# Optimization experiments

Measured on AMD Instinct MI355X. Metric: run time of the kernel, lower is better.

The kernel has to match this reference:

```python
import jax, jax.numpy as jnp
import numpy as np

B, H, W, C = 2, 64, 64, 256
G, K, L = 16, 9, 2
Cg = C // G


def _ln(x, g, b, eps=1e-6):
    m = jnp.mean(x, -1, keepdims=True)
    v = jnp.mean((x - m) ** 2, -1, keepdims=True)
    return (x - m) * jax.lax.rsqrt(v + eps) * g + b


def _conv(x, w, b=None, groups=1):
    y = jax.lax.conv_general_dilated(x, w, (1, 1), 'SAME',
        dimension_numbers=('NHWC', 'HWIO', 'NHWC'), feature_group_count=groups)
    return y if b is None else y + b


def _gelu(x):
    return jax.nn.gelu(x, approximate=False)  # torch nn.GELU (exact erf)


def _dcnv3(x, dw_w, dw_b, dwn_g, dwn_b, off_w, off_b, msk_w, msk_b,
           inp_w, inp_b, out_w, out_b, offset_scale=1.0):
    # x: [B,H,W,C] channels-last. kernel=3, stride=1, pad=1, dilation=1.
    xp = x @ inp_w + inp_b                                   # input_proj
    f = _gelu(_ln(_conv(x, dw_w, dw_b, groups=C), dwn_g, dwn_b))  # dw_conv branch
    off = (f @ off_w + off_b).reshape(B, H, W, G, K, 2) * offset_scale  # pixel units (x,y)
    mask = jax.nn.softmax((f @ msk_w + msk_b).reshape(B, H, W, G, K), axis=-1)
    dy, dx = jnp.meshgrid(jnp.arange(3.0) - 1.0, jnp.arange(3.0) - 1.0, indexing='ij')
    gx = dx.reshape(-1)
    gy = dy.reshape(-1)  # [K] kernel dilation grid
    # sampling locations in the zero-padded (pad=1) frame; pixel i center = i+0.5
    loc_x = (jnp.arange(W, dtype=x.dtype) + 1.5)[None, None, :, None, None] + gx + off[..., 0]
    loc_y = (jnp.arange(H, dtype=x.dtype) + 1.5)[None, :, None, None, None] + gy + off[..., 1]
    xg = jnp.pad(xp, ((0, 0), (1, 1), (1, 1), (0, 0))).reshape(B, H + 2, W + 2, G, Cg)
    px = loc_x - 0.5
    py = loc_y - 0.5
    x0 = jnp.floor(px).astype(jnp.int32)
    y0 = jnp.floor(py).astype(jnp.int32)
    fx = (px - x0)[..., None]
    fy = (py - y0)[..., None]
    Hp, Wp = H + 2, W + 2
    bi = jnp.arange(B).reshape(B, 1, 1, 1, 1)
    gi = jnp.arange(G).reshape(1, 1, 1, G, 1)

    def gather(yi, xi):  # zero padding outside bounds (grid_sample padding_mode='zeros')
        ok = ((yi >= 0) & (yi < Hp) & (xi >= 0) & (xi < Wp)).astype(x.dtype)[..., None]
        return xg[bi, jnp.clip(yi, 0, Hp - 1), jnp.clip(xi, 0, Wp - 1), gi] * ok

    top = gather(y0, x0) * (1 - fx) + gather(y0, x0 + 1) * fx
    bot = gather(y0 + 1, x0) * (1 - fx) + gather(y0 + 1, x0 + 1) * fx
    samp = top * (1 - fy) + bot * fy                         # [B,H,W,G,K,Cg]
    out = (samp * mask[..., None]).sum(4).reshape(B, H, W, C)
    return out @ out_w + out_b                               # output_proj


def _leffn(x, dc_w, dc_b, g, b, c1_w, c1_b, c2_w, c2_b, gamma):
    y = _ln(_conv(x, dc_w, dc_b, groups=C), g, b)
    y = _gelu(y @ c1_w + c1_b) @ c2_w + c2_b
    return x + gamma * y


def _cbam(x, w1, w2, sa_w, g, b):
    fc = lambda v: jax.nn.relu(v @ w1) @ w2
    ca = jax.nn.sigmoid(fc(x.mean((1, 2))) + fc(x.max((1, 2))))[:, None, None, :]
    x = x * ca
    sm = jnp.stack([x.mean(-1), x.max(-1)], -1)              # [B,H,W,2]
    x = x * jax.nn.sigmoid(_conv(sm, sa_w))
    return _ln(x, g, b)


def _upsample(x, w, bb, g, bt):
    y = jax.image.resize(x, (B, 2 * H, 2 * W, C), 'bilinear')  # align_corners=False
    y = _conv(y, w, bb)                                        # 3x3, C -> C//2
    return _gelu(_ln(y, g, bt))


def _forward(x, ln1_g, ln1_b, dw_w, dw_b, dwn_g, dwn_b, off_w, off_b, msk_w, msk_b,
             inp_w, inp_b, out_w, out_b, ln2_g, ln2_b, dc_w, dc_b, fn_g, fn_b,
             c1_w, c1_b, c2_w, c2_b, ffn_gamma, ca_w1, ca_w2, sa_w, cb_g, cb_b,
             nf_g, nf_b, up_w, up_b, up_g, up_bt):
    x = _cbam(x, ca_w1, ca_w2, sa_w, cb_g, cb_b)
    for i in range(L):  # fixed small depth; structural loop
        x = x + _dcnv3(_ln(x, ln1_g[i], ln1_b[i]), dw_w[i], dw_b[i], dwn_g[i], dwn_b[i],
                       off_w[i], off_b[i], msk_w[i], msk_b[i], inp_w[i], inp_b[i],
                       out_w[i], out_b[i])
        x = x + _leffn(_ln(x, ln2_g[i], ln2_b[i]), dc_w[i], dc_b[i], fn_g[i], fn_b[i],
                       c1_w[i], c1_b[i], c2_w[i], c2_b[i], ffn_gamma[i])
    x = _ln(x, nf_g, nf_b)
    return _upsample(x, up_w, up_b, up_g, up_bt)


def setup_inputs() -> dict:
    ks = iter(jax.random.split(jax.random.key(0), 80))
    r = lambda shp, s=0.02: jax.random.normal(next(ks), shp, dtype=jnp.float32) * s
    one = lambda shp: jnp.ones(shp, jnp.float32)
    zero = lambda shp: jnp.zeros(shp, jnp.float32)
    return dict(
        x=jax.random.normal(next(ks), (B, H, W, C), dtype=jnp.float32),
        ln1_g=one((L, C)), ln1_b=zero((L, C)),
        dw_w=r((L, 3, 3, 1, C)), dw_b=zero((L, C)),
        dwn_g=one((L, C)), dwn_b=zero((L, C)),
        off_w=r((L, C, G * K * 2), 0.01), off_b=zero((L, G * K * 2)),
        msk_w=r((L, C, G * K)), msk_b=zero((L, G * K)),
        inp_w=r((L, C, C)), inp_b=zero((L, C)),
        out_w=r((L, C, C)), out_b=zero((L, C)),
        ln2_g=one((L, C)), ln2_b=zero((L, C)),
        dc_w=r((L, 7, 7, 1, C)), dc_b=zero((L, C)),
        fn_g=one((L, C)), fn_b=zero((L, C)),
        c1_w=r((L, C, 4 * C)), c1_b=zero((L, 4 * C)),
        c2_w=r((L, 4 * C, C)), c2_b=zero((L, C)),
        ffn_gamma=0.7 * one((L, C)),
        ca_w1=r((C, C // 16)), ca_w2=r((C // 16, C)),
        sa_w=r((7, 7, 2, 1)),
        cb_g=one((C,)), cb_b=zero((C,)),
        nf_g=one((C,)), nf_b=zero((C,)),
        up_w=r((3, 3, C, C // 2)), up_b=zero((C // 2,)),
        up_g=one((C // 2,)), up_bt=zero((C // 2,)),
    )


def reference(x, ln1_g, ln1_b, dw_w, dw_b, dwn_g, dwn_b, off_w, off_b, msk_w, msk_b,
              inp_w, inp_b, out_w, out_b, ln2_g, ln2_b, dc_w, dc_b, fn_g, fn_b,
              c1_w, c1_b, c2_w, c2_b, ffn_gamma, ca_w1, ca_w2, sa_w, cb_g, cb_b,
              nf_g, nf_b, up_w, up_b, up_g, up_bt):
    return _forward(x, ln1_g, ln1_b, dw_w, dw_b, dwn_g, dwn_b, off_w, off_b, msk_w, msk_b,
                    inp_w, inp_b, out_w, out_b, ln2_g, ln2_b, dc_w, dc_b, fn_g, fn_b,
                    c1_w, c1_b, c2_w, c2_b, ffn_gamma, ca_w1, ca_w2, sa_w, cb_g, cb_b,
                    nf_g, nf_b, up_w, up_b, up_g, up_bt)
```

## Files before the change

### kernel.cpp

```cpp
#include <hip/hip_runtime.h>
#include <math.h>

#define B_ 2
#define H_ 64
#define W_ 64
#define C_ 256
#define G_ 16
#define HW_ (H_*W_)
#define M_ (B_*HW_)
#define C4_ (4*C_)
#define OFFN_ 288
#define MSKN_ 144
#define OMN_ 432
#define UH_ 128
#define UW_ 128
#define MUP_ (B_*UH_*UW_)
#define KUP_ (9*C_)
#define NOUT_ 128

typedef short short8 __attribute__((ext_vector_type(8)));
typedef float f32x4 __attribute__((ext_vector_type(4)));
typedef unsigned short us4 __attribute__((ext_vector_type(4)));

__device__ __forceinline__ float gelu_f(float x){
  return 0.5f * x * (1.f + erff(x * 0.70710678118654752440f));
}
__device__ __forceinline__ float sigmoid_f(float x){ return 1.f/(1.f+expf(-x)); }
__device__ __forceinline__ unsigned short f2bf(float x){
  unsigned int u = __float_as_uint(x);
  unsigned int r = (u + 0x7fffu + ((u>>16)&1u)) >> 16;
  return (unsigned short)r;
}
__device__ __forceinline__ float bf2f(unsigned short u){
  return __uint_as_float(((unsigned int)u) << 16);
}
__device__ __forceinline__ float bfl(unsigned int u){ return __uint_as_float(u<<16); }
__device__ __forceinline__ float bfh(unsigned int u){ return __uint_as_float(u & 0xffff0000u); }
__device__ __forceinline__ unsigned int pk(float a, float b){
  return (unsigned int)f2bf(a) | ((unsigned int)f2bf(b) << 16);
}

__device__ __forceinline__ void block_sum2(float& s, float& ss, float* sm){
  #pragma unroll
  for (int off=32; off>0; off>>=1){ s += __shfl_down(s, off); ss += __shfl_down(ss, off); }
  int lane = threadIdx.x & 63, wid = threadIdx.x >> 6;
  if (lane == 0){ sm[wid] = s; sm[4+wid] = ss; }
  __syncthreads();
  float a = 0.f, b = 0.f;
  int nw = blockDim.x >> 6;
  for (int i=0;i<nw;i++){ a += sm[i]; b += sm[4+i]; }
  s = a; ss = b;
}

__device__ __forceinline__ void block_summax(float& s, float& m, float* sm){
  #pragma unroll
  for (int off=32; off>0; off>>=1){ s += __shfl_down(s, off); m = fmaxf(m, __shfl_down(m, off)); }
  int lane = threadIdx.x & 63, wid = threadIdx.x >> 6;
  if (lane == 0){ sm[wid] = s; sm[4+wid] = m; }
  __syncthreads();
  float a = 0.f, b = -3.4e38f;
  int nw = blockDim.x >> 6;
  for (int i=0;i<nw;i++){ a += sm[i]; b = fmaxf(b, sm[4+i]); }
  s = a; m = b;
}

#define NJOBS 13
struct WtJobs {
  const float* src[NJOBS];
  unsigned short* dst[NJOBS];
  int Kd[NJOBS], Nd[NJOBS];
  int tOff[NJOBS+1];
};

__global__ __launch_bounds__(256) void k_wt_all(WtJobs J){
  __shared__ float tile[32][33];
  int bid = blockIdx.x;
  int j = 0;
  while (bid >= J.tOff[j+1]) j++;
  int lt = bid - J.tOff[j];
  const float* W = J.src[j];
  unsigned short* Wt = J.dst[j];
  int Kd = J.Kd[j], Nd = J.Nd[j];
  int ktiles = Kd >> 5;
  int k0 = (lt % ktiles) * 32, n0 = (lt / ktiles) * 32;
  int t = threadIdx.x;
  int r = t>>3, c4 = (t&7)*4;
  float4 v = make_float4(0.f,0.f,0.f,0.f);
  if (n0 + c4 < Nd) v = *(const float4*)(W + (size_t)(k0+r)*Nd + n0 + c4);
  tile[c4+0][r]=v.x; tile[c4+1][r]=v.y; tile[c4+2][r]=v.z; tile[c4+3][r]=v.w;
  __syncthreads();
  if (n0 + r < Nd){
    us4 o;
    o.x = f2bf(tile[r][c4+0]); o.y = f2bf(tile[r][c4+1]);
    o.z = f2bf(tile[r][c4+2]); o.w = f2bf(tile[r][c4+3]);
    *(us4*)(Wt + (size_t)(n0+r)*Kd + k0 + c4) = o;
  }
}

__global__ __launch_bounds__(256) void k_chpool(const float* __restrict__ Xin,
      float* __restrict__ psum, float* __restrict__ pmax){
  int chunk = blockIdx.x, b = blockIdx.y; int c = threadIdx.x;
  const float* p = Xin + (((size_t)b*HW_) + chunk*32)*C_ + c;
  float s = 0.f, m = -3.4e38f;
  for (int i=0;i<32;i++){ float v = p[(size_t)i*C_]; s += v; m = fmaxf(m, v); }
  psum[(b*128+chunk)*C_+c] = s; pmax[(b*128+chunk)*C_+c] = m;
}

__global__ __launch_bounds__(512) void k_ca(const float* __restrict__ psum, const float* __restrict__ pmax,
    const float* __restrict__ w1, const float* __restrict__ w2, float* __restrict__ ca){
  __shared__ float pm[2][256], px[2][256], hh[2][2][16];
  int t = threadIdx.x;
  {
    int b = t >> 8, c = t & 255;
    float s = 0.f, m = -3.4e38f;
    for (int ch=0; ch<128; ch++){ s += psum[(b*128+ch)*256+c]; m = fmaxf(m, pmax[(b*128+ch)*256+c]); }
    pm[b][c] = s * (1.f/4096.f); px[b][c] = m;
  }
  __syncthreads();
  if (t < 64){
    int b = t >> 5, typ = (t >> 4) & 1, j = t & 15;
    const float* src = typ ? px[b] : pm[b];
    float a = 0.f;
    for (int c2=0;c2<256;c2++) a += src[c2]*w1[c2*16+j];
    hh[b][typ][j] = fmaxf(a, 0.f);
  }
  __syncthreads();
  {
    int b = t >> 8, c = t & 255;
    float a = 0.f;
    for (int j=0;j<16;j++) a += (hh[b][0][j]+hh[b][1][j]) * w2[j*256+c];
    ca[b*256+c] = sigmoid_f(a);
  }
}

__global__ __launch_bounds__(256) void k_apply_ca(const float* __restrict__ Xin, float* __restrict__ X,
    const float* __restrict__ ca, float* __restrict__ smean, float* __restrict__ smax){
  __shared__ float sm[12];
  int pix = blockIdx.x, c = threadIdx.x;
  int b = pix >> 12;
  float v = Xin[(size_t)pix*C_+c] * ca[b*C_+c];
  X[(size_t)pix*C_+c] = v;
  float s = v, m = v;
  block_summax(s, m, sm);
  if (c == 0){ smean[pix] = s * (1.f/C_); smax[pix] = m; }
}

__global__ __launch_bounds__(256) void k_sa(const float* __restrict__ smean, const float* __restrict__ smax,
    const float* __restrict__ w, float* __restrict__ sa){
  int pix = blockIdx.x*256 + threadIdx.x;
  if (pix >= M_) return;
  int b = pix >> 12, hw = pix & 4095, h = hw >> 6, ww = hw & 63;
  float s = 0.f;
  for (int ky=0;ky<7;ky++){
    int hh = h + ky - 3; if (hh < 0 || hh >= H_) continue;
    for (int kx=0;kx<7;kx++){
      int xx = ww + kx - 3; if (xx < 0 || xx >= W_) continue;
      int q = (b<<12) + (hh<<6) + xx;
      s += smean[q]*w[(ky*7+kx)*2+0] + smax[q]*w[(ky*7+kx)*2+1];
    }
  }
  sa[pix] = sigmoid_f(s);
}

__global__ __launch_bounds__(256) void k_mul_ln(float* __restrict__ X, const float* __restrict__ sa,
    const float* __restrict__ g, const float* __restrict__ b){
  __shared__ float sm[12];
  int pix = blockIdx.x, c = threadIdx.x;
  float v = X[(size_t)pix*C_+c] * sa[pix];
  float s = v, ss = v*v;
  block_sum2(s, ss, sm);
  float mean = s * (1.f/C_), var = ss*(1.f/C_) - mean*mean;
  float r = rsqrtf(var + 1e-6f);
  X[(size_t)pix*C_+c] = (v-mean)*r*g[c] + b[c];
}

__global__ __launch_bounds__(256) void k_ln(const float* __restrict__ In, float* __restrict__ Out,
    unsigned short* __restrict__ Outb, const float* __restrict__ g, const float* __restrict__ b){
  __shared__ float sm[12];
  int pix = blockIdx.x, c = threadIdx.x;
  float v = In[(size_t)pix*C_+c];
  float s = v, ss = v*v;
  block_sum2(s, ss, sm);
  float mean = s * (1.f/C_), var = ss*(1.f/C_) - mean*mean;
  float r = rsqrtf(var + 1e-6f);
  float o = (v-mean)*r*g[c] + b[c];
  if (Out)  Out[(size_t)pix*C_+c] = o;
  if (Outb) Outb[(size_t)pix*C_+c] = f2bf(o);
}

template<int KS, int DOGELU>
__global__ __launch_bounds__(256) void k_dwconv(const unsigned short* __restrict__ T,
    unsigned short* __restrict__ Out,
    const float* __restrict__ w, const float* __restrict__ bias,
    const float* __restrict__ g, const float* __restrict__ bb){
  constexpr int R = KS/2;
  int t = blockIdx.x*256 + threadIdx.x;
  int pix = t >> 5, grp = t & 31;
  int c0 = grp*8;
  int b = pix >> 12, hw = pix & 4095, h = hw >> 6, ww = hw & 63;
  float acc[8];
  {
    float4 b0 = *(const float4*)(bias + c0), b1 = *(const float4*)(bias + c0 + 4);
    acc[0]=b0.x; acc[1]=b0.y; acc[2]=b0.z; acc[3]=b0.w;
    acc[4]=b1.x; acc[5]=b1.y; acc[6]=b1.z; acc[7]=b1.w;
  }
  const unsigned short* tb = T + ((size_t)b*HW_)*C_ + c0;
  for (int ky=0;ky<KS;ky++){
    int hh = h + ky - R; if (hh < 0 || hh >= H_) continue;
    for (int kx=0;kx<KS;kx++){
      int xx = ww + kx - R; if (xx < 0 || xx >= W_) continue;
      uint4 a = *(const uint4*)(tb + ((size_t)hh*W_+xx)*C_);
      const float* wp = w + (ky*KS+kx)*C_ + c0;
      float4 w0 = *(const float4*)wp, w1 = *(const float4*)(wp+4);
      acc[0] += bfl(a.x)*w0.x; acc[1] += bfh(a.x)*w0.y;
      acc[2] += bfl(a.y)*w0.z; acc[3] += bfh(a.y)*w0.w;
      acc[4] += bfl(a.z)*w1.x; acc[5] += bfh(a.z)*w1.y;
      acc[6] += bfl(a.w)*w1.z; acc[7] += bfh(a.w)*w1.w;
    }
  }
  float s = 0.f, ss = 0.f;
  #pragma unroll
  for (int i=0;i<8;i++){ s += acc[i]; ss += acc[i]*acc[i]; }
  #pragma unroll
  for (int off=1; off<32; off<<=1){ s += __shfl_xor(s, off); ss += __shfl_xor(ss, off); }
  float mean = s * (1.f/C_), var = ss*(1.f/C_) - mean*mean;
  float r = rsqrtf(var + 1e-6f);
  float4 g0 = *(const float4*)(g + c0), g1 = *(const float4*)(g + c0 + 4);
  float4 p0 = *(const float4*)(bb + c0), p1 = *(const float4*)(bb + c0 + 4);
  float o[8];
  o[0]=(acc[0]-mean)*r*g0.x+p0.x; o[1]=(acc[1]-mean)*r*g0.y+p0.y;
  o[2]=(acc[2]-mean)*r*g0.z+p0.z; o[3]=(acc[3]-mean)*r*g0.w+p0.w;
  o[4]=(acc[4]-mean)*r*g1.x+p1.x; o[5]=(acc[5]-mean)*r*g1.y+p1.y;
  o[6]=(acc[6]-mean)*r*g1.z+p1.z; o[7]=(acc[7]-mean)*r*g1.w+p1.w;
  if (DOGELU){
    #pragma unroll
    for (int i=0;i<8;i++) o[i] = gelu_f(o[i]);
  }
  uint4 ov;
  ov.x = pk(o[0],o[1]); ov.y = pk(o[2],o[3]); ov.z = pk(o[4],o[5]); ov.w = pk(o[6],o[7]);
  *(uint4*)(Out + (size_t)pix*C_ + c0) = ov;
}

template<int TM, int EP, int OUTBF>
__global__ __launch_bounds__(256) void k_gemm_mfma(
    const unsigned short* __restrict__ A, const unsigned short* __restrict__ Bt,
    void* __restrict__ OutV, const float* __restrict__ bias,
    const float* __restrict__ res1, const float* __restrict__ res2,
    const float* __restrict__ gamma, int Ni, int Ki)
{
  constexpr int LD = 40;
  __shared__ unsigned short As[TM*LD];
  __shared__ unsigned short Bs[128*LD];
  const int tid = threadIdx.x;
  const int wave = tid >> 6, lane = tid & 63;
  const int m0 = blockIdx.x * TM, n0 = blockIdx.y * 128;
  const int wm0 = (wave >> 1) * (TM/2);
  const int wn0 = (wave & 1) * 64;
  constexpr int MI = TM/32;
  f32x4 acc[MI][4] = {};
  const int lm = lane & 15, kq = lane >> 4;
  constexpr int ACH = TM*4/256;

  for (int k0 = 0; k0 < Ki; k0 += 32){
    #pragma unroll
    for (int i=0;i<ACH;i++){
      int ch = tid*ACH + i;
      int r = ch >> 2, cc = (ch & 3) * 8;
      short8 v = *(const short8*)(A + (size_t)(m0 + r)*Ki + k0 + cc);
      *(short8*)(As + r*LD + cc) = v;
    }
    #pragma unroll
    for (int i=0;i<2;i++){
      int ch = tid + 256*i;
      int r = ch >> 2, cc = (ch & 3) * 8;
      short8 v = {};
      if (n0 + r < Ni) v = *(const short8*)(Bt + (size_t)(n0 + r)*Ki + k0 + cc);
      *(short8*)(Bs + r*LD + cc) = v;
    }
    __syncthreads();
    short8 af[MI], bf[4];
    #pragma unroll
    for (int mi=0;mi<MI;mi++) af[mi] = *(const short8*)(As + (wm0 + mi*16 + lm)*LD + kq*8);
    #pragma unroll
    for (int ni=0;ni<4;ni++)  bf[ni] = *(const short8*)(Bs + (wn0 + ni*16 + lm)*LD + kq*8);
    #pragma unroll
    for (int mi=0;mi<MI;mi++)
      #pragma unroll
      for (int ni=0;ni<4;ni++)
        acc[mi][ni] = __builtin_amdgcn_mfma_f32_16x16x32_bf16(af[mi], bf[ni], acc[mi][ni], 0,0,0);
    __syncthreads();
  }
  #pragma unroll
  for (int mi=0;mi<MI;mi++){
    #pragma unroll
    for (int ni=0;ni<4;ni++){
      int n = n0 + wn0 + ni*16 + lm;
      if (n < Ni){
        float bv;
        if constexpr (EP==4) bv = (n < OFFN_) ? bias[n] : res1[n-OFFN_];
        else bv = bias[n];
        #pragma unroll
        for (int r=0;r<4;r++){
          int m = m0 + wm0 + mi*16 + kq*4 + r;
          size_t o = (size_t)m*Ni + n;
          float v = acc[mi][ni][r] + bv;
          if constexpr (EP==1) v = gelu_f(v);
          if constexpr (EP==2) v = res1[o] + v;
          if constexpr (EP==3) v = res1[o] + res2[o] + gamma[n]*v;
          if constexpr (OUTBF) ((unsigned short*)OutV)[o] = f2bf(v);
          else                 ((float*)OutV)[o] = v;
        }
      }
    }
  }
}

__global__ __launch_bounds__(256) void k_dcn(const unsigned short* __restrict__ xp,
    const float* __restrict__ OM, unsigned short* __restrict__ S){
  __shared__ float lom[16*OMN_];
  int pix0 = blockIdx.x * 16;
  {
    const float* gsrc = OM + (size_t)pix0*OMN_;
    for (int idx = threadIdx.x; idx < 16*OMN_; idx += 256) lom[idx] = gsrc[idx];
  }
  __syncthreads();
  int pl = threadIdx.x >> 4, g = threadIdx.x & 15;
  int pix = pix0 + pl;
  int b = pix >> 12, hw = pix & 4095, h = hw >> 6, ww = hw & 63;
  const float* offp = lom + pl*OMN_ + g*18;
  const float* mp   = lom + pl*OMN_ + OFFN_ + g*9;
  const unsigned short* xpb = xp + ((size_t)b*HW_)*C_ + g*16;
  float e[9]; float mx = -3.4e38f;
  #pragma unroll
  for (int k=0;k<9;k++){ e[k] = mp[k]; mx = fmaxf(mx, e[k]); }
  float ssum = 0.f;
  #pragma unroll
  for (int k=0;k<9;k++){ e[k] = expf(e[k]-mx); ssum += e[k]; }
  float rinv = 1.f/ssum;
  float acc[16] = {};
  #pragma unroll
  for (int k=0;k<9;k++){
    float ox = offp[k*2+0], oy = offp[k*2+1];
    float px = (float)(ww + (k%3)) + ox;
    float py = (float)(h  + (k/3)) + oy;
    int x0 = (int)floorf(px), y0 = (int)floorf(py);
    float fx = px - (float)x0, fy = py - (float)y0;
    float mk = e[k]*rinv;
    float w00 = mk*(1.f-fx)*(1.f-fy), w01 = mk*fx*(1.f-fy);
    float w10 = mk*(1.f-fx)*fy,       w11 = mk*fx*fy;
    #define CORNER(yy,xx,WGT) do{ \
      if ((yy)>=1 && (yy)<=H_ && (xx)>=1 && (xx)<=W_){ \
        const unsigned short* p = xpb + ((size_t)((yy)-1)*W_ + ((xx)-1))*C_; \
        uint4 a0 = *(const uint4*)p; uint4 a1 = *(const uint4*)(p+8); \
        acc[0]+=WGT*bfl(a0.x); acc[1]+=WGT*bfh(a0.x); acc[2]+=WGT*bfl(a0.y); acc[3]+=WGT*bfh(a0.y); \
        acc[4]+=WGT*bfl(a0.z); acc[5]+=WGT*bfh(a0.z); acc[6]+=WGT*bfl(a0.w); acc[7]+=WGT*bfh(a0.w); \
        acc[8]+=WGT*bfl(a1.x); acc[9]+=WGT*bfh(a1.x); acc[10]+=WGT*bfl(a1.y); acc[11]+=WGT*bfh(a1.y); \
        acc[12]+=WGT*bfl(a1.z); acc[13]+=WGT*bfh(a1.z); acc[14]+=WGT*bfl(a1.w); acc[15]+=WGT*bfh(a1.w); \
      } \
    }while(0)
    CORNER(y0,   x0,   w00);
    CORNER(y0,   x0+1, w01);
    CORNER(y0+1, x0,   w10);
    CORNER(y0+1, x0+1, w11);
    #undef CORNER
  }
  unsigned short* sp = S + (size_t)pix*C_ + g*16;
  uint4 o0, o1;
  o0.x = pk(acc[0],acc[1]);   o0.y = pk(acc[2],acc[3]);
  o0.z = pk(acc[4],acc[5]);   o0.w = pk(acc[6],acc[7]);
  o1.x = pk(acc[8],acc[9]);   o1.y = pk(acc[10],acc[11]);
  o1.z = pk(acc[12],acc[13]); o1.w = pk(acc[14],acc[15]);
  *(uint4*)sp = o0;
  *(uint4*)(sp+8) = o1;
}

__global__ __launch_bounds__(256) void k_upsample(const unsigned short* __restrict__ T, unsigned short* __restrict__ U){
  int t = blockIdx.x*256 + threadIdx.x;
  int opix = t >> 5, grp = t & 31;
  int c0 = grp*8;
  int ox = opix & 127, oy = (opix >> 7) & 127, b = opix >> 14;
  float sy = oy*0.5f - 0.25f, sx = ox*0.5f - 0.25f;
  int y0 = (int)floorf(sy), x0 = (int)floorf(sx);
  float fy = sy - (float)y0, fx = sx - (float)x0;
  int y0c = min(max(y0,0),H_-1), y1c = min(max(y0+1,0),H_-1);
  int x0c = min(max(x0,0),W_-1), x1c = min(max(x0+1,0),W_-1);
  const unsigned short* tb = T + ((size_t)b*HW_)*C_ + c0;
  uint4 q00 = *(const uint4*)(tb + ((size_t)y0c*W_+x0c)*C_);
  uint4 q01 = *(const uint4*)(tb + ((size_t)y0c*W_+x1c)*C_);
  uint4 q10 = *(const uint4*)(tb + ((size_t)y1c*W_+x0c)*C_);
  uint4 q11 = *(const uint4*)(tb + ((size_t)y1c*W_+x1c)*C_);
  float w00=(1.f-fy)*(1.f-fx), w01=(1.f-fy)*fx, w10=fy*(1.f-fx), w11=fy*fx;
  float o[8];
  o[0]=w00*bfl(q00.x)+w01*bfl(q01.x)+w10*bfl(q10.x)+w11*bfl(q11.x);
  o[1]=w00*bfh(q00.x)+w01*bfh(q01.x)+w10*bfh(q10.x)+w11*bfh(q11.x);
  o[2]=w00*bfl(q00.y)+w01*bfl(q01.y)+w10*bfl(q10.y)+w11*bfl(q11.y);
  o[3]=w00*bfh(q00.y)+w01*bfh(q01.y)+w10*bfh(q10.y)+w11*bfh(q11.y);
  o[4]=w00*bfl(q00.z)+w01*bfl(q01.z)+w10*bfl(q10.z)+w11*bfl(q11.z);
  o[5]=w00*bfh(q00.z)+w01*bfh(q01.z)+w10*bfh(q10.z)+w11*bfh(q11.z);
  o[6]=w00*bfl(q00.w)+w01*bfl(q01.w)+w10*bfl(q10.w)+w11*bfl(q11.w);
  o[7]=w00*bfh(q00.w)+w01*bfh(q01.w)+w10*bfh(q10.w)+w11*bfh(q11.w);
  uint4 ov;
  ov.x = pk(o[0],o[1]); ov.y = pk(o[2],o[3]); ov.z = pk(o[4],o[5]); ov.w = pk(o[6],o[7]);
  *(uint4*)(U + (size_t)opix*C_ + c0) = ov;
}

__global__ __launch_bounds__(256) void k_upconv_mfma(
    const unsigned short* __restrict__ U, const unsigned short* __restrict__ Wt,
    float* __restrict__ Out, const float* __restrict__ bias)
{
  constexpr int LD = 40;
  __shared__ unsigned short As[64*LD];
  __shared__ unsigned short Bs[128*LD];
  const int tid = threadIdx.x;
  const int wave = tid >> 6, lane = tid & 63;
  const int m0 = blockIdx.x * 64;
  const int wm0 = (wave >> 1) * 32;
  const int wn0 = (wave & 1) * 64;
  f32x4 acc[2][4] = {};
  const int lm = lane & 15, kq = lane >> 4;
  const int ar = tid >> 2, ac = (tid & 3) * 8;
  const int ma = m0 + ar;
  const int ba = ma >> 14, oya = (ma >> 7) & 127, oxa = ma & 127;

  for (int k0 = 0; k0 < KUP_; k0 += 32){
    int tap = k0 >> 8, cc0 = k0 & 255;
    int dy = tap/3 - 1, dx = tap%3 - 1;
    {
      int iy = oya + dy, ix = oxa + dx;
      short8 v = {};
      if (iy >= 0 && iy < UH_ && ix >= 0 && ix < UW_)
        v = *(const short8*)(U + (((size_t)ba*UH_ + iy)*UW_ + ix)*C_ + cc0 + ac);
      *(short8*)(As + ar*LD + ac) = v;
    }
    #pragma unroll
    for (int i=0;i<2;i++){
      int ch = tid + 256*i;
      int r = ch >> 2, cc = (ch & 3) * 8;
      short8 v = *(const short8*)(Wt + (size_t)r*KUP_ + k0 + cc);
      *(short8*)(Bs + r*LD + cc) = v;
    }
    __syncthreads();
    short8 af[2], bf[4];
    #pragma unroll
    for (int mi=0;mi<2;mi++) af[mi] = *(const short8*)(As + (wm0 + mi*16 + lm)*LD + kq*8);
    #pragma unroll
    for (int ni=0;ni<4;ni++) bf[ni] = *(const short8*)(Bs + (wn0 + ni*16 + lm)*LD + kq*8);
    #pragma unroll
    for (int mi=0;mi<2;mi++)
      #pragma unroll
      for (int ni=0;ni<4;ni++)
        acc[mi][ni] = __builtin_amdgcn_mfma_f32_16x16x32_bf16(af[mi], bf[ni], acc[mi][ni], 0,0,0);
    __syncthreads();
  }
  #pragma unroll
  for (int mi=0;mi<2;mi++){
    #pragma unroll
    for (int ni=0;ni<4;ni++){
      int n = wn0 + ni*16 + lm;
      float bv = bias[n];
      #pragma unroll
      for (int r=0;r<4;r++){
        int m = m0 + wm0 + mi*16 + kq*4 + r;
        Out[(size_t)m*NOUT_ + n] = acc[mi][ni][r] + bv;
      }
    }
  }
}

__global__ __launch_bounds__(128) void k_out_ln_gelu(const float* __restrict__ In, float* __restrict__ Out,
    const float* __restrict__ g, const float* __restrict__ b){
  __shared__ float sm[12];
  int pix = blockIdx.x, c = threadIdx.x;
  float v = In[(size_t)pix*NOUT_ + c];
  float s = v, ss = v*v;
  block_sum2(s, ss, sm);
  float mean = s * (1.f/NOUT_), var = ss*(1.f/NOUT_) - mean*mean;
  float r = rsqrtf(var + 1e-6f);
  Out[(size_t)pix*NOUT_ + c] = gelu_f((v-mean)*r*g[c] + b[c]);
}

extern "C" void kernel_launch(void* const* d_in, const int* in_sizes, int n_in,
                              void* d_out, int out_size, void* d_ws, size_t ws_size,
                              hipStream_t stream)
{
  (void)in_sizes; (void)n_in; (void)out_size; (void)ws_size;
  const float* x_in = (const float*)d_in[0];
  char* w = (char*)d_ws;
  const size_t MB = 1u<<20;
  float* X    = (float*)(w + 0*MB);
  float* T    = (float*)(w + 8*MB);
  float* OM   = (float*)(w + 16*MB);
  unsigned short* MIDb = (unsigned short*)(w + 30*MB);
  unsigned short* Ub   = MIDb;
  unsigned short* Tb   = (unsigned short*)(w + 46*MB);
  unsigned short* Fb   = (unsigned short*)(w + 50*MB);
  unsigned short* XPb  = (unsigned short*)(w + 54*MB);
  unsigned short* DW7b = (unsigned short*)(w + 58*MB);
  unsigned short* Sb   = (unsigned short*)(w + 62*MB);
  unsigned short* WT   = (unsigned short*)(w + 66*MB);
  float* C2   = (float*)(w + 0*MB);
  float* psum = (float*)(w + 70*MB);
  float* pmax = psum + 65536;
  float* ca   = pmax + 65536;
  float* smean= ca + 512;
  float* smax = smean + 8192;
  float* sa   = smax + 8192;

  unsigned short* WtInp[2], *WtOut[2], *WtOM[2], *WtC1[2], *WtC2[2];
  {
    size_t o = 0;
    for (int i=0;i<2;i++){
      WtInp[i] = WT + o; o += 65536;
      WtOut[i] = WT + o; o += 65536;
      WtOM[i]  = WT + o; o += 110592;
      WtC1[i]  = WT + o; o += 262144;
      WtC2[i]  = WT + o; o += 262144;
    }
  }
  unsigned short* WtUp = WT + 1531904;

  WtJobs J;
  {
    int ji = 0, toff = 0;
    auto add = [&](const float* s, unsigned short* d, int Kd, int Nd){
      J.src[ji]=s; J.dst[ji]=d; J.Kd[ji]=Kd; J.Nd[ji]=Nd;
      J.tOff[ji]=toff; toff += (Kd>>5) * ((Nd+31)>>5); ji++;
    };
    for (int i=0;i<2;i++){
      add((const float*)d_in[11] + (size_t)i*C_*C_,   WtInp[i], C_, C_);
      add((const float*)d_in[13] + (size_t)i*C_*C_,   WtOut[i], C_, C_);
      add((const float*)d_in[7]  + (size_t)i*C_*OFFN_, WtOM[i], C_, OFFN_);
      add((const float*)d_in[9]  + (size_t)i*C_*MSKN_, WtOM[i] + (size_t)OFFN_*C_, C_, MSKN_);
      add((const float*)d_in[21] + (size_t)i*C_*C4_,  WtC1[i], C_, C4_);
      add((const float*)d_in[23] + (size_t)i*C4_*C_,  WtC2[i], C4_, C_);
    }
    add((const float*)d_in[33], WtUp, KUP_, NOUT_);
    J.tOff[ji] = toff;
    k_wt_all<<<toff,256,0,stream>>>(J);
  }

  k_chpool<<<dim3(128,2),256,0,stream>>>(x_in, psum, pmax);
  k_ca<<<1,512,0,stream>>>(psum, pmax, (const float*)d_in[26], (const float*)d_in[27], ca);
  k_apply_ca<<<M_,256,0,stream>>>(x_in, X, ca, smean, smax);
  k_sa<<<M_/256,256,0,stream>>>(smean, smax, (const float*)d_in[28], sa);
  k_mul_ln<<<M_,256,0,stream>>>(X, sa, (const float*)d_in[29], (const float*)d_in[30]);

  for (int i=0;i<2;i++){
    const float* ln1g = (const float*)d_in[1] + i*C_;
    const float* ln1b = (const float*)d_in[2] + i*C_;
    const float* dww  = (const float*)d_in[3] + i*9*C_;
    const float* dwb  = (const float*)d_in[4] + i*C_;
    const float* dwng = (const float*)d_in[5] + i*C_;
    const float* dwnb = (const float*)d_in[6] + i*C_;
    const float* offb = (const float*)d_in[8] + i*OFFN_;
    const float* mskb = (const float*)d_in[10] + i*MSKN_;
    const float* inpb = (const float*)d_in[12] + i*C_;
    const float* outb = (const float*)d_in[14] + i*C_;
    const float* ln2g = (const float*)d_in[15] + i*C_;
    const float* ln2b = (const float*)d_in[16] + i*C_;
    const float* dcw  = (const float*)d_in[17] + i*49*C_;
    const float* dcb  = (const float*)d_in[18] + i*C_;
    const float* fng  = (const float*)d_in[19] + i*C_;
    const float* fnb  = (const float*)d_in[20] + i*C_;
    const float* c1b  = (const float*)d_in[22] + i*C4_;
    const float* c2b  = (const float*)d_in[24] + i*C_;
    const float* gam  = (const float*)d_in[25] + i*C_;

    k_ln<<<M_,256,0,stream>>>(X, nullptr, Tb, ln1g, ln1b);
    k_gemm_mfma<64,0,1><<<dim3(M_/64,2),256,0,stream>>>(Tb, WtInp[i], XPb, inpb, nullptr,nullptr,nullptr, C_, C_);
    k_dwconv<3,1><<<M_*32/256,256,0,stream>>>(Tb, Fb, dww, dwb, dwng, dwnb);
    k_gemm_mfma<64,4,0><<<dim3(M_/64,4),256,0,stream>>>(Fb, WtOM[i], OM, offb, mskb, nullptr,nullptr, OMN_, C_);
    k_dcn<<<M_/16,256,0,stream>>>(XPb, OM, Sb);
    k_gemm_mfma<64,2,0><<<dim3(M_/64,2),256,0,stream>>>(Sb, WtOut[i], X, outb, X, nullptr, nullptr, C_, C_);

    k_ln<<<M_,256,0,stream>>>(X, T, Tb, ln2g, ln2b);
    k_dwconv<7,0><<<M_*32/256,256,0,stream>>>(Tb, DW7b, dcw, dcb, fng, fnb);
    k_gemm_mfma<128,1,1><<<dim3(M_/128,8),256,0,stream>>>(DW7b, WtC1[i], MIDb, c1b, nullptr,nullptr,nullptr, C4_, C_);
    k_gemm_mfma<64,3,0><<<dim3(M_/64,2),256,0,stream>>>(MIDb, WtC2[i], X, c2b, X, T, gam, C_, C4_);
  }

  k_ln<<<M_,256,0,stream>>>(X, nullptr, Tb, (const float*)d_in[31], (const float*)d_in[32]);
  k_upsample<<<MUP_*32/256,256,0,stream>>>(Tb, Ub);
  k_upconv_mfma<<<MUP_/64,256,0,stream>>>(Ub, WtUp, C2, (const float*)d_in[34]);
  k_out_ln_gelu<<<MUP_,128,0,stream>>>(C2, (float*)d_out, (const float*)d_in[35], (const float*)d_in[36]);
}
```

Before: 548.3 us.

## Fuse LayerNorms into GEMM epilogues and the upconv output kernel

The standalone LayerNorm kernels are removed. A new full-row GEMM (32x256 tile) applies the residual add and then a row LayerNorm in its epilogue, writing both the fp32 residual stream and the bf16 normalized input for the next stage. The first ln1 is merged into the spatial-attention mul+LN kernel. The upconv GEMM now steps K by 64 and applies the final LN+GELU in its epilogue. These cut extra kernel launches and full-tensor round trips through memory. In exchange, the new GEMM runs fewer blocks, each loading the whole weight tile, and the FFN residual now reads a bf16 copy instead of fp32, which slightly lowers precision.

```diff
diff --git a/kernel.cpp b/kernel.cpp
--- a/kernel.cpp
+++ b/kernel.cpp
@@ -162,8 +162,9 @@
   sa[pix] = sigmoid_f(s);
 }
 
-__global__ __launch_bounds__(256) void k_mul_ln(float* __restrict__ X, const float* __restrict__ sa,
-    const float* __restrict__ g, const float* __restrict__ b){
+__global__ __launch_bounds__(256) void k_mul_ln_ln1(float* __restrict__ X, const float* __restrict__ sa,
+    const float* __restrict__ g, const float* __restrict__ b,
+    const float* __restrict__ g1, const float* __restrict__ b1, unsigned short* __restrict__ Tb){
   __shared__ float sm[12];
   int pix = blockIdx.x, c = threadIdx.x;
   float v = X[(size_t)pix*C_+c] * sa[pix];
@@ -171,21 +172,14 @@
   block_sum2(s, ss, sm);
   float mean = s * (1.f/C_), var = ss*(1.f/C_) - mean*mean;
   float r = rsqrtf(var + 1e-6f);
-  X[(size_t)pix*C_+c] = (v-mean)*r*g[c] + b[c];
-}
-
-__global__ __launch_bounds__(256) void k_ln(const float* __restrict__ In, float* __restrict__ Out,
-    unsigned short* __restrict__ Outb, const float* __restrict__ g, const float* __restrict__ b){
-  __shared__ float sm[12];
-  int pix = blockIdx.x, c = threadIdx.x;
-  float v = In[(size_t)pix*C_+c];
-  float s = v, ss = v*v;
+  float x0 = (v-mean)*r*g[c] + b[c];
+  X[(size_t)pix*C_+c] = x0;
+  __syncthreads();
+  s = x0; ss = x0*x0;
   block_sum2(s, ss, sm);
-  float mean = s * (1.f/C_), var = ss*(1.f/C_) - mean*mean;
-  float r = rsqrtf(var + 1e-6f);
-  float o = (v-mean)*r*g[c] + b[c];
-  if (Out)  Out[(size_t)pix*C_+c] = o;
-  if (Outb) Outb[(size_t)pix*C_+c] = f2bf(o);
+  mean = s * (1.f/C_); var = ss*(1.f/C_) - mean*mean;
+  r = rsqrtf(var + 1e-6f);
+  Tb[(size_t)pix*C_+c] = f2bf((x0-mean)*r*g1[c] + b1[c]);
 }
 
 template<int KS, int DOGELU>
@@ -245,8 +239,7 @@
 __global__ __launch_bounds__(256) void k_gemm_mfma(
     const unsigned short* __restrict__ A, const unsigned short* __restrict__ Bt,
     void* __restrict__ OutV, const float* __restrict__ bias,
-    const float* __restrict__ res1, const float* __restrict__ res2,
-    const float* __restrict__ gamma, int Ni, int Ki)
+    const float* __restrict__ bias2, int Ni, int Ki)
 {
   constexpr int LD = 40;
   __shared__ unsigned short As[TM*LD];
@@ -265,14 +258,14 @@
     #pragma unroll
     for (int i=0;i<ACH;i++){
       int ch = tid*ACH + i;
-      int r = ch >> 2, cc = (ch & 3) * 8;
+      int r = ch >> 2, cc = (ch & 3) << 3;
       short8 v = *(const short8*)(A + (size_t)(m0 + r)*Ki + k0 + cc);
       *(short8*)(As + r*LD + cc) = v;
     }
     #pragma unroll
     for (int i=0;i<2;i++){
       int ch = tid + 256*i;
-      int r = ch >> 2, cc = (ch & 3) * 8;
+      int r = ch >> 2, cc = (ch & 3) << 3;
       short8 v = {};
       if (n0 + r < Ni) v = *(const short8*)(Bt + (size_t)(n0 + r)*Ki + k0 + cc);
       *(short8*)(Bs + r*LD + cc) = v;
@@ -297,7 +290,7 @@
       int n = n0 + wn0 + ni*16 + lm;
       if (n < Ni){
         float bv;
-        if constexpr (EP==4) bv = (n < OFFN_) ? bias[n] : res1[n-OFFN_];
+        if constexpr (EP==4) bv = (n < OFFN_) ? bias[n] : bias2[n-OFFN_];
         else bv = bias[n];
         #pragma unroll
         for (int r=0;r<4;r++){
@@ -305,12 +298,107 @@
           size_t o = (size_t)m*Ni + n;
           float v = acc[mi][ni][r] + bv;
           if constexpr (EP==1) v = gelu_f(v);
-          if constexpr (EP==2) v = res1[o] + v;
-          if constexpr (EP==3) v = res1[o] + res2[o] + gamma[n]*v;
           if constexpr (OUTBF) ((unsigned short*)OutV)[o] = f2bf(v);
           else                 ((float*)OutV)[o] = v;
         }
       }
+    }
+  }
+}
+
+template<int EP>
+__global__ __launch_bounds__(256) void k_gemm_ln(
+    const unsigned short* __restrict__ A, const unsigned short* __restrict__ Bt,
+    float* __restrict__ X, const float* __restrict__ bias,
+    const unsigned short* __restrict__ res2b, const float* __restrict__ gamma,
+    unsigned short* __restrict__ OutTb,
+    const float* __restrict__ lng, const float* __restrict__ lnb, int Ki)
+{
+  constexpr int LD = 40;
+  __shared__ unsigned short As[32*LD];
+  __shared__ unsigned short Bs[256*LD];
+  __shared__ float rs[32][2], rq[32][2];
+  const int tid = threadIdx.x;
+  const int wave = tid >> 6, lane = tid & 63;
+  const int m0 = blockIdx.x * 32;
+  const int wm0 = (wave >> 1) * 16;
+  const int wn0 = (wave & 1) * 128;
+  const int lm = lane & 15, kq = lane >> 4;
+  f32x4 acc[8] = {};
+
+  for (int k0 = 0; k0 < Ki; k0 += 32){
+    if (tid < 128){
+      int r = tid >> 2, cc = (tid & 3) << 3;
+      short8 v = *(const short8*)(A + (size_t)(m0 + r)*Ki + k0 + cc);
+      *(short8*)(As + r*LD + cc) = v;
+    }
+    #pragma unroll
+    for (int i=0;i<4;i++){
+      int ch = tid + 256*i;
+      int r = ch >> 2, cc = (ch & 3) << 3;
+      short8 v = *(const short8*)(Bt + (size_t)r*Ki + k0 + cc);
+      *(short8*)(Bs + r*LD + cc) = v;
+    }
+    __syncthreads();
+    short8 af = *(const short8*)(As + (wm0 + lm)*LD + kq*8);
+    short8 bf[8];
+    #pragma unroll
+    for (int ni=0;ni<8;ni++) bf[ni] = *(const short8*)(Bs + (wn0 + ni*16 + lm)*LD + kq*8);
+    #pragma unroll
+    for (int ni=0;ni<8;ni++)
+      acc[ni] = __builtin_amdgcn_mfma_f32_16x16x32_bf16(af, bf[ni], acc[ni], 0,0,0);
+    __syncthreads();
+  }
+  int nn[8]; float bv[8], gv[8];
+  #pragma unroll
+  for (int ni=0;ni<8;ni++){
+    nn[ni] = wn0 + ni*16 + lm;
+    bv[ni] = bias[nn[ni]];
+    if constexpr (EP==3) gv[ni] = gamma[nn[ni]];
+  }
+  float ps[4] = {}, pq[4] = {};
+  #pragma unroll
+  for (int r=0;r<4;r++){
+    int m = m0 + wm0 + kq*4 + r;
+    #pragma unroll
+    for (int ni=0;ni<8;ni++){
+      size_t o = (size_t)m*C_ + nn[ni];
+      float v = acc[ni][r] + bv[ni];
+      if constexpr (EP==2) v = X[o] + v;
+      if constexpr (EP==3) v = X[o] + bf2f(res2b[o]) + gv[ni]*v;
+      X[o] = v;
+      acc[ni][r] = v;
+      ps[r] += v; pq[r] += v*v;
+    }
+  }
+  #pragma unroll
+  for (int off=1; off<16; off<<=1){
+    #pragma unroll
+    for (int r=0;r<4;r++){ ps[r] += __shfl_xor(ps[r], off); pq[r] += __shfl_xor(pq[r], off); }
+  }
+  if (lm == 0){
+    #pragma unroll
+    for (int r=0;r<4;r++){
+      rs[wm0 + kq*4 + r][wave & 1] = ps[r];
+      rq[wm0 + kq*4 + r][wave & 1] = pq[r];
+    }
+  }
+  __syncthreads();
+  float lg[8], lb[8];
+  #pragma unroll
+  for (int ni=0;ni<8;ni++){ lg[ni] = lng[nn[ni]]; lb[ni] = lnb[nn[ni]]; }
+  #pragma unroll
+  for (int r=0;r<4;r++){
+    int row = wm0 + kq*4 + r;
+    int m = m0 + row;
+    float s = rs[row][0] + rs[row][1];
+    float q = rq[row][0] + rq[row][1];
+    float mean = s * (1.f/C_), var = q*(1.f/C_) - mean*mean;
+    float rstd = rsqrtf(var + 1e-6f);
+    #pragma unroll
+    for (int ni=0;ni<8;ni++){
+      size_t o = (size_t)m*C_ + nn[ni];
+      OutTb[o] = f2bf((acc[ni][r]-mean)*rstd*lg[ni] + lb[ni]);
     }
   }
 }
@@ -404,79 +492,116 @@
   *(uint4*)(U + (size_t)opix*C_ + c0) = ov;
 }
 
-__global__ __launch_bounds__(256) void k_upconv_mfma(
+__global__ __launch_bounds__(256) void k_upconv_ln(
     const unsigned short* __restrict__ U, const unsigned short* __restrict__ Wt,
-    float* __restrict__ Out, const float* __restrict__ bias)
+    float* __restrict__ Out, const float* __restrict__ bias,
+    const float* __restrict__ g, const float* __restrict__ bb)
 {
-  constexpr int LD = 40;
+  constexpr int LD = 72;
   __shared__ unsigned short As[64*LD];
   __shared__ unsigned short Bs[128*LD];
+  __shared__ float rs[64][2], rq[64][2];
   const int tid = threadIdx.x;
   const int wave = tid >> 6, lane = tid & 63;
   const int m0 = blockIdx.x * 64;
   const int wm0 = (wave >> 1) * 32;
   const int wn0 = (wave & 1) * 64;
+  const int lm = lane & 15, kq = lane >> 4;
   f32x4 acc[2][4] = {};
-  const int lm = lane & 15, kq = lane >> 4;
-  const int ar = tid >> 2, ac = (tid & 3) * 8;
-  const int ma = m0 + ar;
-  const int ba = ma >> 14, oya = (ma >> 7) & 127, oxa = ma & 127;
-
-  for (int k0 = 0; k0 < KUP_; k0 += 32){
+  const int r0 = tid >> 3, cA = (tid & 7) << 3;
+  int bar[2], oyr[2], oxr[2];
+  #pragma unroll
+  for (int i=0;i<2;i++){
+    int m = m0 + r0 + 32*i;
+    bar[i] = m >> 14; oyr[i] = (m >> 7) & 127; oxr[i] = m & 127;
+  }
+
+  for (int k0 = 0; k0 < KUP_; k0 += 64){
     int tap = k0 >> 8, cc0 = k0 & 255;
     int dy = tap/3 - 1, dx = tap%3 - 1;
-    {
-      int iy = oya + dy, ix = oxa + dx;
+    #pragma unroll
+    for (int i=0;i<2;i++){
+      int iy = oyr[i] + dy, ix = oxr[i] + dx;
       short8 v = {};
       if (iy >= 0 && iy < UH_ && ix >= 0 && ix < UW_)
-        v = *(const short8*)(U + (((size_t)ba*UH_ + iy)*UW_ + ix)*C_ + cc0 + ac);
-      *(short8*)(As + ar*LD + ac) = v;
-    }
-    #pragma unroll
-    for (int i=0;i<2;i++){
-      int ch = tid + 256*i;
-      int r = ch >> 2, cc = (ch & 3) * 8;
-      short8 v = *(const short8*)(Wt + (size_t)r*KUP_ + k0 + cc);
-      *(short8*)(Bs + r*LD + cc) = v;
+        v = *(const short8*)(U + (((size_t)bar[i]*UH_ + iy)*UW_ + ix)*C_ + cc0 + cA);
+      *(short8*)(As + (r0 + 32*i)*LD + cA) = v;
+    }
+    #pragma unroll
+    for (int i=0;i<4;i++){
+      int r = r0 + 32*i;
+      short8 v = *(const short8*)(Wt + (size_t)r*KUP_ + k0 + cA);
+      *(short8*)(Bs + r*LD + cA) = v;
     }
     __syncthreads();
-    short8 af[2], bf[4];
-    #pragma unroll
-    for (int mi=0;mi<2;mi++) af[mi] = *(const short8*)(As + (wm0 + mi*16 + lm)*LD + kq*8);
-    #pragma unroll
-    for (int ni=0;ni<4;ni++) bf[ni] = *(const short8*)(Bs + (wn0 + ni*16 + lm)*LD + kq*8);
+    short8 af[2][2], bf[4][2];
     #pragma unroll
     for (int mi=0;mi<2;mi++)
       #pragma unroll
-      for (int ni=0;ni<4;ni++)
-        acc[mi][ni] = __builtin_amdgcn_mfma_f32_16x16x32_bf16(af[mi], bf[ni], acc[mi][ni], 0,0,0);
+      for (int kk=0;kk<2;kk++)
+        af[mi][kk] = *(const short8*)(As + (wm0 + mi*16 + lm)*LD + kk*32 + kq*8);
+    #pragma unroll
+    for (int ni=0;ni<4;ni++)
+      #pragma unroll
+      for (int kk=0;kk<2;kk++)
+        bf[ni][kk] = *(const short8*)(Bs + (wn0 + ni*16 + lm)*LD + kk*32 + kq*8);
+    #pragma unroll
+    for (int kk=0;kk<2;kk++)
+      #pragma unroll
+      for (int mi=0;mi<2;mi++)
+        #pragma unroll
+        for (int ni=0;ni<4;ni++)
+          acc[mi][ni] = __builtin_amdgcn_mfma_f32_16x16x32_bf16(af[mi][kk], bf[ni][kk], acc[mi][ni], 0,0,0);
     __syncthreads();
   }
-  #pragma unroll
-  for (int mi=0;mi<2;mi++){
-    #pragma unroll
-    for (int ni=0;ni<4;ni++){
-      int n = wn0 + ni*16 + lm;
-      float bv = bias[n];
+  int nn[4]; float bv[4];
+  #pragma unroll
+  for (int ni=0;ni<4;ni++){ nn[ni] = wn0 + ni*16 + lm; bv[ni] = bias[nn[ni]]; }
+  float ps[2][4] = {}, pq[2][4] = {};
+  #pragma unroll
+  for (int mi=0;mi<2;mi++)
+    #pragma unroll
+    for (int r=0;r<4;r++)
+      #pragma unroll
+      for (int ni=0;ni<4;ni++){
+        float v = acc[mi][ni][r] + bv[ni];
+        acc[mi][ni][r] = v;
+        ps[mi][r] += v; pq[mi][r] += v*v;
+      }
+  #pragma unroll
+  for (int off=1; off<16; off<<=1){
+    #pragma unroll
+    for (int mi=0;mi<2;mi++)
+      #pragma unroll
+      for (int r=0;r<4;r++){ ps[mi][r] += __shfl_xor(ps[mi][r], off); pq[mi][r] += __shfl_xor(pq[mi][r], off); }
+  }
+  if (lm == 0){
+    #pragma unroll
+    for (int mi=0;mi<2;mi++)
       #pragma unroll
       for (int r=0;r<4;r++){
-        int m = m0 + wm0 + mi*16 + kq*4 + r;
-        Out[(size_t)m*NOUT_ + n] = acc[mi][ni][r] + bv;
+        rs[wm0 + mi*16 + kq*4 + r][wave & 1] = ps[mi][r];
+        rq[wm0 + mi*16 + kq*4 + r][wave & 1] = pq[mi][r];
       }
-    }
-  }
-}
-
-__global__ __launch_bounds__(128) void k_out_ln_gelu(const float* __restrict__ In, float* __restrict__ Out,
-    const float* __restrict__ g, const float* __restrict__ b){
-  __shared__ float sm[12];
-  int pix = blockIdx.x, c = threadIdx.x;
-  float v = In[(size_t)pix*NOUT_ + c];
-  float s = v, ss = v*v;
-  block_sum2(s, ss, sm);
-  float mean = s * (1.f/NOUT_), var = ss*(1.f/NOUT_) - mean*mean;
-  float r = rsqrtf(var + 1e-6f);
-  Out[(size_t)pix*NOUT_ + c] = gelu_f((v-mean)*r*g[c] + b[c]);
+  }
+  __syncthreads();
+  float gv[4], pv[4];
+  #pragma unroll
+  for (int ni=0;ni<4;ni++){ gv[ni] = g[nn[ni]]; pv[ni] = bb[nn[ni]]; }
+  #pragma unroll
+  for (int mi=0;mi<2;mi++)
+    #pragma unroll
+    for (int r=0;r<4;r++){
+      int row = wm0 + mi*16 + kq*4 + r;
+      int m = m0 + row;
+      float s = rs[row][0] + rs[row][1];
+      float q = rq[row][0] + rq[row][1];
+      float mean = s * (1.f/NOUT_), var = q*(1.f/NOUT_) - mean*mean;
+      float rstd = rsqrtf(var + 1e-6f);
+      #pragma unroll
+      for (int ni=0;ni<4;ni++)
+        Out[(size_t)m*NOUT_ + nn[ni]] = gelu_f((acc[mi][ni][r]-mean)*rstd*gv[ni] + pv[ni]);
+    }
 }
 
 extern "C" void kernel_launch(void* const* d_in, const int* in_sizes, int n_in,
@@ -488,18 +613,16 @@
   char* w = (char*)d_ws;
   const size_t MB = 1u<<20;
   float* X    = (float*)(w + 0*MB);
-  float* T    = (float*)(w + 8*MB);
-  float* OM   = (float*)(w + 16*MB);
-  unsigned short* MIDb = (unsigned short*)(w + 30*MB);
+  float* OM   = (float*)(w + 8*MB);
+  unsigned short* MIDb = (unsigned short*)(w + 22*MB);
   unsigned short* Ub   = MIDb;
-  unsigned short* Tb   = (unsigned short*)(w + 46*MB);
-  unsigned short* Fb   = (unsigned short*)(w + 50*MB);
-  unsigned short* XPb  = (unsigned short*)(w + 54*MB);
-  unsigned short* DW7b = (unsigned short*)(w + 58*MB);
-  unsigned short* Sb   = (unsigned short*)(w + 62*MB);
-  unsigned short* WT   = (unsigned short*)(w + 66*MB);
-  float* C2   = (float*)(w + 0*MB);
-  float* psum = (float*)(w + 70*MB);
+  unsigned short* Tb   = (unsigned short*)(w + 38*MB);
+  unsigned short* Fb   = (unsigned short*)(w + 42*MB);
+  unsigned short* XPb  = (unsigned short*)(w + 46*MB);
+  unsigned short* DW7b = (unsigned short*)(w + 50*MB);
+  unsigned short* Sb   = (unsigned short*)(w + 54*MB);
+  unsigned short* WT   = (unsigned short*)(w + 58*MB);
+  float* psum = (float*)(w + 62*MB);
   float* pmax = psum + 65536;
   float* ca   = pmax + 65536;
   float* smean= ca + 512;
@@ -543,11 +666,10 @@
   k_ca<<<1,512,0,stream>>>(psum, pmax, (const float*)d_in[26], (const float*)d_in[27], ca);
   k_apply_ca<<<M_,256,0,stream>>>(x_in, X, ca, smean, smax);
   k_sa<<<M_/256,256,0,stream>>>(smean, smax, (const float*)d_in[28], sa);
-  k_mul_ln<<<M_,256,0,stream>>>(X, sa, (const float*)d_in[29], (const float*)d_in[30]);
+  k_mul_ln_ln1<<<M_,256,0,stream>>>(X, sa, (const float*)d_in[29], (const float*)d_in[30],
+      (const float*)d_in[1], (const float*)d_in[2], Tb);
 
   for (int i=0;i<2;i++){
-    const float* ln1g = (const float*)d_in[1] + i*C_;
-    const float* ln1b = (const float*)d_in[2] + i*C_;
     const float* dww  = (const float*)d_in[3] + i*9*C_;
     const float* dwb  = (const float*)d_in[4] + i*C_;
     const float* dwng = (const float*)d_in[5] + i*C_;
@@ -565,22 +687,21 @@
     const float* c1b  = (const float*)d_in[22] + i*C4_;
     const float* c2b  = (const float*)d_in[24] + i*C_;
     const float* gam  = (const float*)d_in[25] + i*C_;
-
-    k_ln<<<M_,256,0,stream>>>(X, nullptr, Tb, ln1g, ln1b);
-    k_gemm_mfma<64,0,1><<<dim3(M_/64,2),256,0,stream>>>(Tb, WtInp[i], XPb, inpb, nullptr,nullptr,nullptr, C_, C_);
+    const float* nxg = (i==0) ? (const float*)d_in[1] + C_ : (const float*)d_in[31];
+    const float* nxb = (i==0) ? (const float*)d_in[2] + C_ : (const float*)d_in[32];
+
+    k_gemm_mfma<64,0,1><<<dim3(M_/64,2),256,0,stream>>>(Tb, WtInp[i], XPb, inpb, nullptr, C_, C_);
     k_dwconv<3,1><<<M_*32/256,256,0,stream>>>(Tb, Fb, dww, dwb, dwng, dwnb);
-    k_gemm_mfma<64,4,0><<<dim3(M_/64,4),256,0,stream>>>(Fb, WtOM[i], OM, offb, mskb, nullptr,nullptr, OMN_, C_);
+    k_gemm_mfma<64,4,0><<<dim3(M_/64,4),256,0,stream>>>(Fb, WtOM[i], OM, offb, mskb, OMN_, C_);
     k_dcn<<<M_/16,256,0,stream>>>(XPb, OM, Sb);
-    k_gemm_mfma<64,2,0><<<dim3(M_/64,2),256,0,stream>>>(Sb, WtOut[i], X, outb, X, nullptr, nullptr, C_, C_);
-
-    k_ln<<<M_,256,0,stream>>>(X, T, Tb, ln2g, ln2b);
+    k_gemm_ln<2><<<M_/32,256,0,stream>>>(Sb, WtOut[i], X, outb, nullptr, nullptr, Tb, ln2g, ln2b, C_);
+
     k_dwconv<7,0><<<M_*32/256,256,0,stream>>>(Tb, DW7b, dcw, dcb, fng, fnb);
-    k_gemm_mfma<128,1,1><<<dim3(M_/128,8),256,0,stream>>>(DW7b, WtC1[i], MIDb, c1b, nullptr,nullptr,nullptr, C4_, C_);
-    k_gemm_mfma<64,3,0><<<dim3(M_/64,2),256,0,stream>>>(MIDb, WtC2[i], X, c2b, X, T, gam, C_, C4_);
-  }
-
-  k_ln<<<M_,256,0,stream>>>(X, nullptr, Tb, (const float*)d_in[31], (const float*)d_in[32]);
+    k_gemm_mfma<128,1,1><<<dim3(M_/128,8),256,0,stream>>>(DW7b, WtC1[i], MIDb, c1b, nullptr, C4_, C_);
+    k_gemm_ln<3><<<M_/32,256,0,stream>>>(MIDb, WtC2[i], X, c2b, Tb, gam, Tb, nxg, nxb, C4_);
+  }
+
   k_upsample<<<MUP_*32/256,256,0,stream>>>(Tb, Ub);
-  k_upconv_mfma<<<MUP_/64,256,0,stream>>>(Ub, WtUp, C2, (const float*)d_in[34]);
-  k_out_ln_gelu<<<MUP_,128,0,stream>>>(C2, (float*)d_out, (const float*)d_in[35], (const float*)d_in[36]);
-}
+  k_upconv_ln<<<MUP_/64,256,0,stream>>>(Ub, WtUp, (float*)d_out, (const float*)d_in[34],
+      (const float*)d_in[35], (const float*)d_in[36]);
+}
```

After: 520.5 us. 1.05x faster.
